# Kernel optimization log

Measured on AMD Instinct MI355X. Metric: run time of the kernel, lower is better.

The kernel has to match this reference:

```python
import jax, jax.numpy as jnp
import numpy as np

N_TYPES = 2
N_NODES = 50000
N_EDGES = 400000
C = 128
H = 4
D = C // H
L = 2
# edge type e connects src node type META[e][0] -> dst node type META[e][1]
META = ((0, 1), (1, 0))


def setup_inputs() -> dict:
    key = jax.random.key(0)
    ks = jax.random.split(key, 16)
    s = 0.05
    return {
        "x": jax.random.normal(ks[0], (N_TYPES, N_NODES, C), jnp.float32),
        "edge_index": jax.random.randint(ks[1], (2, 2, N_EDGES), 0, N_NODES, jnp.int64),
        "Wk": jax.random.normal(ks[2], (L, N_TYPES, C, C), jnp.float32) * s,
        "bk": jax.random.normal(ks[3], (L, N_TYPES, C), jnp.float32) * s,
        "Wq": jax.random.normal(ks[4], (L, N_TYPES, C, C), jnp.float32) * s,
        "bq": jax.random.normal(ks[5], (L, N_TYPES, C), jnp.float32) * s,
        "Wv": jax.random.normal(ks[6], (L, N_TYPES, C, C), jnp.float32) * s,
        "bv": jax.random.normal(ks[7], (L, N_TYPES, C), jnp.float32) * s,
        "Wa": jax.random.normal(ks[8], (L, N_TYPES, C, C), jnp.float32) * s,
        "ba": jax.random.normal(ks[9], (L, N_TYPES, C), jnp.float32) * s,
        "skip": jax.random.normal(ks[10], (L, N_TYPES), jnp.float32),
        "a_rel": jax.random.normal(ks[11], (L, 2, H, D, D), jnp.float32) * s,
        "m_rel": jax.random.normal(ks[12], (L, 2, H, D, D), jnp.float32) * s,
        "p_rel": jnp.ones((L, 2, H), jnp.float32),
        "ln_g": jnp.ones((L, N_TYPES, C), jnp.float32),
        "ln_b": jnp.zeros((L, N_TYPES, C), jnp.float32),
    }


def _layer(x, edge_index, Wk, bk, Wq, bq, Wv, bv, Wa, ba, skip, a_rel, m_rel, p_rel, ln_g, ln_b):
    # x: [T, N, C] ; per-type K/Q/V projections -> [T, N, H, D]
    k = (jnp.einsum('tnc,tcd->tnd', x, Wk) + bk[:, None]).reshape(N_TYPES, N_NODES, H, D)
    q = (jnp.einsum('tnc,tcd->tnd', x, Wq) + bq[:, None]).reshape(N_TYPES, N_NODES, H, D)
    v = (jnp.einsum('tnc,tcd->tnd', x, Wv) + bv[:, None]).reshape(N_TYPES, N_NODES, H, D)
    scale = 1.0 / float(np.sqrt(D))
    out = jnp.zeros((N_TYPES, N_NODES, H, D), x.dtype)
    for e, (st, dt) in enumerate(META):
        si, di = edge_index[e, 0], edge_index[e, 1]
        # per-relation transforms of gathered src keys/values: [E, H, D]
        k_rel = jnp.einsum('ehd,hdf->ehf', k[st][si], a_rel[e])
        v_rel = jnp.einsum('ehd,hdf->ehf', v[st][si], m_rel[e])
        # attention logits [E, H], softmax grouped by destination node
        att = jnp.sum(q[dt][di] * k_rel, axis=-1) * p_rel[e] * scale
        amax = jax.ops.segment_max(att, di, num_segments=N_NODES)
        att = jnp.exp(att - amax[di])
        den = jax.ops.segment_sum(att, di, num_segments=N_NODES)
        att = att / (den[di] + 1e-16)
        agg = jax.ops.segment_sum(att[..., None] * v_rel, di, num_segments=N_NODES)
        out = out.at[dt].add(agg)
    o = out.reshape(N_TYPES, N_NODES, C)
    o = jnp.einsum('tnc,tcd->tnd', jax.nn.gelu(o), Wa) + ba[:, None]
    beta = jax.nn.sigmoid(skip)[:, None, None]
    x = beta * o + (1.0 - beta) * x
    # per-type LayerNorm over features, then ReLU
    mu = jnp.mean(x, axis=-1, keepdims=True)
    var = jnp.var(x, axis=-1, keepdims=True)
    x = (x - mu) * jax.lax.rsqrt(var + 1e-5) * ln_g[:, None] + ln_b[:, None]
    return jax.nn.relu(x)


def reference(x, edge_index, Wk, bk, Wq, bq, Wv, bv, Wa, ba, skip, a_rel, m_rel, p_rel, ln_g, ln_b):
    for l in range(L):
        x = _layer(x, edge_index, Wk[l], bk[l], Wq[l], bq[l], Wv[l], bv[l],
                   Wa[l], ba[l], skip[l], a_rel[l], m_rel[l], p_rel[l], ln_g[l], ln_b[l])
    # x_dict[entity_table]: return node type 0 ("user") embeddings
    return x[0]
```

## Files before the change

### kernel.cpp

```cpp
#include <hip/hip_runtime.h>

#define NN 50000
#define EE 400000
#define CC 128
#define TT 2
#define NT16R 3128
#define KPB 8
#define SCB ((NN + 1023) / 1024)
#define EB ((EE + 256 * KPB - 1) / (256 * KPB))
#define CVTB (NT16R / 4)
#define PREPN (2 * 384 * 128 + 2 * 128 * 128 + 2 * 384)
#define PREPB ((PREPN + 255) / 256)
#define GB ((NN + 31) / 32)

typedef float floatx4 __attribute__((ext_vector_type(4)));
typedef float floatx2 __attribute__((ext_vector_type(2)));
typedef _Float16 half8 __attribute__((ext_vector_type(8)));
typedef _Float16 half2t __attribute__((ext_vector_type(2)));

__device__ __forceinline__ unsigned pk2h(float a, float b) {
    return __builtin_bit_cast(unsigned, __builtin_amdgcn_cvt_pkrtz(a, b));
}
__device__ __forceinline__ float gelu_f(float x) {
    float u = 0.7978845608028654f * (x + 0.044715f * x * x * x);
    float t = __expf(2.f * u);
    return x * (1.f - 1.f / (t + 1.f));
}

__device__ __forceinline__ floatx2 pkfma(floatx2 a, floatx2 b, floatx2 c) {
#if __has_builtin(__builtin_elementwise_fma)
    return __builtin_elementwise_fma(a, b, c);
#else
    floatx2 r;
    r.x = fmaf(a.x, b.x, c.x);
    r.y = fmaf(a.y, b.y, c.y);
    return r;
#endif
}

__device__ __forceinline__ unsigned pk_fp8x4(float a, float b, float c, float d) {
#if __has_builtin(__builtin_amdgcn_cvt_pk_fp8_f32)
    int v = 0;
    v = __builtin_amdgcn_cvt_pk_fp8_f32(a, b, v, false);
    v = __builtin_amdgcn_cvt_pk_fp8_f32(c, d, v, true);
    return (unsigned)v;
#else
    auto enc = [](float x) -> unsigned {
        unsigned u = __float_as_uint(x);
        unsigned s = (u >> 24) & 0x80;
        int e = (int)((u >> 23) & 0xff);
        unsigned m = u & 0x7fffff;
        if (e == 0) return s;
        int ne = e - 127 + 7;
        if (ne <= 0) {
            unsigned full = (1u << 23) | m;
            int sh = 21 - ne;
            if (sh > 24) return s;
            unsigned r = full >> sh;
            unsigned rem = full & ((1u << sh) - 1);
            unsigned half = 1u << (sh - 1);
            if (rem > half || (rem == half && (r & 1))) r++;
            return s | (r & 0x7f);
        }
        unsigned r = m >> 20;
        unsigned rem = m & 0xfffff;
        if (rem > 0x80000 || (rem == 0x80000 && (r & 1))) {
            r++;
            if (r == 8) { r = 0; ne++; }
        }
        if (ne > 15) return s | 0x7e;
        return s | ((unsigned)ne << 3) | r;
    };
    return enc(a) | (enc(b) << 8) | (enc(c) << 16) | (enc(d) << 24);
#endif
}

template <bool HI>
__device__ __forceinline__ floatx2 upk_fp8(unsigned v) {
#if __has_builtin(__builtin_amdgcn_cvt_pk_f32_fp8)
    return __builtin_amdgcn_cvt_pk_f32_fp8((int)v, HI);
#else
    auto dec = [](unsigned b) -> float {
        unsigned s = b & 0x80;
        unsigned e = (b >> 3) & 0xf;
        unsigned m = b & 7;
        float val;
        if (e == 0) val = (float)m * (1.f / 512.f);
        else val = (1.f + (float)m * 0.125f) * exp2f((float)e - 7.f);
        return s ? -val : val;
    };
    unsigned base = HI ? (v >> 16) : v;
    floatx2 r;
    r.x = dec(base & 0xff);
    r.y = dec((base >> 8) & 0xff);
    return r;
#endif
}

__device__ __forceinline__ int detect_is64(const int* __restrict__ ei, int* sflag) {
    if (threadIdx.x == 0) {
        int orv = 0;
#pragma unroll
        for (int i = 1; i < 64; i += 2) orv |= ei[i];
        *sflag = (orv == 0) ? 1 : 0;
    }
    __syncthreads();
    return *sflag;
}

__device__ __forceinline__ void count_body(const int* __restrict__ ei,
                                           int* __restrict__ counts,
                                           unsigned short* __restrict__ rank,
                                           int e, int bx, int* sflag) {
    int is64 = detect_is64(ei, sflag);
    int tid = threadIdx.x;
    int base = bx * (256 * KPB);
    const size_t db = (size_t)(e * 2 + 1) * EE;
    int di[KPB];
    bool val[KPB];
#pragma unroll
    for (int k = 0; k < KPB; k++) {
        int j = base + k * 256 + tid;
        val[k] = j < EE;
        int jc = val[k] ? j : 0;
        int d = is64 ? ei[(db + jc) * 2] : ei[db + jc];
        di[k] = min(max(d, 0), NN - 1);
    }
    int rk[KPB];
#pragma unroll
    for (int k = 0; k < KPB; k++)
        rk[k] = val[k] ? atomicAdd(&counts[e * NN + di[k]], 1) : 0;
#pragma unroll
    for (int k = 0; k < KPB; k++) {
        int j = base + k * 256 + tid;
        if (val[k]) rank[(size_t)e * EE + j] = (unsigned short)rk[k];
    }
}

__device__ __forceinline__ void scatter_body(const int* __restrict__ ei,
                                             const int* __restrict__ rowptr,
                                             const unsigned short* __restrict__ rank,
                                             int* __restrict__ csr,
                                             int e, int bx, int* sflag) {
    int is64 = detect_is64(ei, sflag);
    int tid = threadIdx.x;
    int base = bx * (256 * KPB);
    const size_t sb = (size_t)(e * 2 + 0) * EE;
    const size_t db = (size_t)(e * 2 + 1) * EE;
    int si[KPB], di[KPB], rk[KPB];
#pragma unroll
    for (int k = 0; k < KPB; k++) {
        int j = base + k * 256 + tid;
        int jc = (j < EE) ? j : 0;
        si[k] = is64 ? ei[(sb + jc) * 2] : ei[sb + jc];
        di[k] = is64 ? ei[(db + jc) * 2] : ei[db + jc];
        rk[k] = rank[(size_t)e * EE + jc];
    }
    int pos[KPB];
#pragma unroll
    for (int k = 0; k < KPB; k++) {
        di[k] = min(max(di[k], 0), NN - 1);
        si[k] = min(max(si[k], 0), NN - 1);
    }
#pragma unroll
    for (int k = 0; k < KPB; k++) pos[k] = rowptr[e * (NN + 1) + di[k]] + rk[k];
#pragma unroll
    for (int k = 0; k < KPB; k++) {
        int j = base + k * 256 + tid;
        if (j < EE) csr[(size_t)e * EE + pos[k]] = si[k];
    }
}

__device__ __forceinline__ void cvt_body(const float* __restrict__ x,
                                         _Float16* __restrict__ xs,
                                         int t, int bx, _Float16* sm) {
    int tid = threadIdx.x;
    int node0 = bx * 64;
#pragma unroll
    for (int p = 0; p < 8; p++) {
        int c = p * 256 + tid;
        int row = c >> 5, ch = c & 31;
        int node = min(node0 + row, NN - 1);
        float4 v = *(const float4*)(x + ((size_t)t * NN + node) * CC + ch * 4);
        uint2 o;
        o.x = pk2h(v.x, v.y);
        o.y = pk2h(v.z, v.w);
        *(uint2*)(sm + row * 132 + ch * 4) = o;
    }
    __syncthreads();
    _Float16* xt = xs + (size_t)t * NT16R * 2048;
#pragma unroll
    for (int p = 0; p < 4; p++) {
        int c = p * 256 + tid;
        int tl = c >> 8, kt = (c >> 6) & 3, l = c & 63;
        int q = l >> 4, ln = l & 15;
        *(uint4*)(xt + ((size_t)(bx * 4 + tl) * 4 + kt) * 512 + l * 8) =
            *(const uint4*)(sm + (tl * 16 + ln) * 132 + kt * 32 + q * 8);
    }
}

__device__ __forceinline__ void prep_body(
    const float* __restrict__ Wk, const float* __restrict__ Wq,
    const float* __restrict__ Wv, const float* __restrict__ Wa,
    const float* __restrict__ bk, const float* __restrict__ bq,
    const float* __restrict__ bv,
    const float* __restrict__ a_rel, const float* __restrict__ m_rel,
    const float* __restrict__ p_rel,
    _Float16* __restrict__ W2, _Float16* __restrict__ Wa2,
    float* __restrict__ beff, int l, int idx) {
    const float SCALE = 0.17677669529663687f * 1.4426950408889634f;
    if (idx < 2 * 384 * 128) {
        int t = idx / (384 * 128);
        int r = idx - t * 384 * 128;
        int n = r >> 7, k = r & 127;
        float val;
        if (n < 128) {
            val = Wq[((l * 2 + t) * 128 + k) * 128 + n] *
                  p_rel[(l * 2 + (1 - t)) * 4 + (n >> 5)] * SCALE;
        } else if (n < 256) {
            int nn = n - 128, h = nn >> 5, f = nn & 31;
            const float* wr = Wk + ((l * 2 + t) * 128 + k) * 128 + h * 32;
            const float* ar = a_rel + (((l * 2 + t) * 4 + h) * 32) * 32 + f;
            float s = 0.f;
            for (int d = 0; d < 32; d++) s += wr[d] * ar[d * 32];
            val = s;
        } else {
            int nn = n - 256, h = nn >> 5, f = nn & 31;
            const float* wr = Wv + ((l * 2 + t) * 128 + k) * 128 + h * 32;
            const float* mr = m_rel + (((l * 2 + t) * 4 + h) * 32) * 32 + f;
            float s = 0.f;
            for (int d = 0; d < 32; d++) s += wr[d] * mr[d * 32];
            val = s;
        }
        W2[(((size_t)(l * 2 + t) * 24 + (n >> 4)) * 4 + (k >> 5)) * 512 +
           (((k & 31) >> 3) * 16 + (n & 15)) * 8 + (k & 7)] = (_Float16)val;
    } else if (idx < 2 * 384 * 128 + 2 * 128 * 128) {
        int r = idx - 2 * 384 * 128;
        int t = r / (128 * 128);
        r -= t * 128 * 128;
        int n = r >> 7, k = r & 127;
        float val = Wa[((l * 2 + t) * 128 + k) * 128 + n];
        Wa2[(((size_t)(l * 2 + t) * 8 + (n >> 4)) * 4 + (k >> 5)) * 512 +
            (((k & 31) >> 3) * 16 + (n & 15)) * 8 + (k & 7)] = (_Float16)val;
    } else if (idx < PREPN) {
        int r = idx - (2 * 384 * 128 + 2 * 128 * 128);
        int t = r / 384, n = r - t * 384;
        float val;
        if (n < 128) {
            val = bq[(l * 2 + t) * 128 + n] * p_rel[(l * 2 + (1 - t)) * 4 + (n >> 5)] * SCALE;
        } else if (n < 256) {
            int nn = n - 128, h = nn >> 5, f = nn & 31;
            float s = 0.f;
            for (int d = 0; d < 32; d++)
                s += bk[(l * 2 + t) * 128 + h * 32 + d] *
                     a_rel[(((l * 2 + t) * 4 + h) * 32 + d) * 32 + f];
            val = s;
        } else {
            int nn = n - 256, h = nn >> 5, f = nn & 31;
            float s = 0.f;
            for (int d = 0; d < 32; d++)
                s += bv[(l * 2 + t) * 128 + h * 32 + d] *
                     m_rel[(((l * 2 + t) * 4 + h) * 32 + d) * 32 + f];
            val = s;
        }
        beff[(l * 2 + t) * 384 + n] = val;
    }
}

__global__ __launch_bounds__(256) void k_fuse_pre(
    const int* __restrict__ ei, int* __restrict__ counts,
    unsigned short* __restrict__ rank,
    const float* __restrict__ x, _Float16* __restrict__ xs,
    const float* __restrict__ Wk, const float* __restrict__ Wq,
    const float* __restrict__ Wv, const float* __restrict__ Wa,
    const float* __restrict__ bk, const float* __restrict__ bq,
    const float* __restrict__ bv,
    const float* __restrict__ a_rel, const float* __restrict__ m_rel,
    const float* __restrict__ p_rel,
    _Float16* __restrict__ W2, _Float16* __restrict__ Wa2,
    float* __restrict__ beff) {
    __shared__ _Float16 sm[64 * 132];
    __shared__ int sflag;
    if (blockIdx.x < EB) {
        count_body(ei, counts, rank, blockIdx.y, blockIdx.x, &sflag);
    } else if (blockIdx.x < EB + CVTB) {
        cvt_body(x, xs, blockIdx.y, blockIdx.x - EB, sm);
    } else {
        prep_body(Wk, Wq, Wv, Wa, bk, bq, bv, a_rel, m_rel, p_rel, W2, Wa2, beff,
                  blockIdx.y, (blockIdx.x - EB - CVTB) * 256 + (int)threadIdx.x);
    }
}

__global__ __launch_bounds__(256) void k_scan1(const int* __restrict__ counts,
                                               int* __restrict__ rowptr,
                                               int* __restrict__ bsum) {
    int e = blockIdx.y, b = blockIdx.x;
    int tid = threadIdx.x, lane = tid & 63, wid = tid >> 6;
    __shared__ int wsum[4];
    int base = b * 1024 + tid * 4;
    int v[4], s = 0;
#pragma unroll
    for (int k2 = 0; k2 < 4; k2++) {
        int i = base + k2;
        v[k2] = (i < NN) ? counts[e * NN + i] : 0;
        s += v[k2];
    }
    int incl = s;
#pragma unroll
    for (int off = 1; off < 64; off <<= 1) {
        int t2 = __shfl_up(incl, off);
        if (lane >= off) incl += t2;
    }
    if (lane == 63) wsum[wid] = incl;
    __syncthreads();
    int woff = 0;
    for (int w2 = 0; w2 < wid; w2++) woff += wsum[w2];
    int excl = woff + incl - s;
#pragma unroll
    for (int k2 = 0; k2 < 4; k2++) {
        int i = base + k2;
        if (i < NN) rowptr[e * (NN + 1) + i] = excl;
        excl += v[k2];
    }
    if (tid == 255) bsum[e * SCB + b] = woff + incl;
}

__global__ __launch_bounds__(256) void k_scan23(int* __restrict__ rowptr,
                                                const int* __restrict__ bsum) {
    __shared__ int soff2[2];
    int e = blockIdx.y, b = blockIdx.x;
    int tid = threadIdx.x, lane = tid & 63, wv = tid >> 6;
    if (wv == 0) {
        int v = (lane < SCB) ? bsum[e * SCB + lane] : 0;
        int incl = v;
#pragma unroll
        for (int off = 1; off < 64; off <<= 1) {
            int t2 = __shfl_up(incl, off);
            if (lane >= off) incl += t2;
        }
        if (lane == b) soff2[0] = incl - v;
        if (lane == SCB - 1) soff2[1] = incl;
    }
    __syncthreads();
    int off = soff2[0];
    int base = b * 1024 + tid * 4;
#pragma unroll
    for (int k2 = 0; k2 < 4; k2++) {
        int i = base + k2;
        if (i < NN) rowptr[e * (NN + 1) + i] += off;
    }
    if (b == 0 && tid == 0) rowptr[e * (NN + 1) + NN] = soff2[1];
}

template <int NT, int COL0>
__device__ __forceinline__ void gemm_body(const _Float16* __restrict__ xs,
                                          const _Float16* __restrict__ W2,
                                          const float* __restrict__ beff,
                                          unsigned char* __restrict__ qkv8,
                                          int l, int t, int bx,
                                          unsigned char* tile) {
    constexpr int RB = (NT == 6) ? 512 : 256;
    constexpr int RS = RB + 16;
    int tid = threadIdx.x;
    int wid = tid >> 6, lane = tid & 63;
    int quad = lane >> 4, ln = lane & 15;
    int node0 = bx * 32;
    int tile0 = bx * 2;
    int lt = l * 2 + t;
    const _Float16* Wt = W2 + (size_t)lt * 24 * 2048;
    const _Float16* xt = xs + (size_t)t * NT16R * 2048;
    half8 bf[2][4];
#pragma unroll
    for (int ns = 0; ns < 2; ns++)
#pragma unroll
        for (int kt = 0; kt < 4; kt++)
            bf[ns][kt] = *(const half8*)(xt + ((size_t)(tile0 + ns) * 4 + kt) * 512 + lane * 8);
    floatx4 acc[NT][2];
#pragma unroll
    for (int nt = 0; nt < NT; nt++)
#pragma unroll
        for (int ns = 0; ns < 2; ns++) acc[nt][ns] = (floatx4){0.f, 0.f, 0.f, 0.f};
#pragma unroll
    for (int nt = 0; nt < NT; nt++) {
        int mt = COL0 / 16 + wid * NT + nt;
#pragma unroll
        for (int kt = 0; kt < 4; kt++) {
            half8 af = *(const half8*)(Wt + ((size_t)mt * 4 + kt) * 512 + lane * 8);
            acc[nt][0] = __builtin_amdgcn_mfma_f32_16x16x32_f16(af, bf[0][kt], acc[nt][0], 0, 0, 0);
            acc[nt][1] = __builtin_amdgcn_mfma_f32_16x16x32_f16(af, bf[1][kt], acc[nt][1], 0, 0, 0);
        }
    }
#pragma unroll
    for (int nt = 0; nt < NT; nt++) {
        int c0 = COL0 + wid * NT * 16 + nt * 16 + quad * 4;
        float4 b4 = *(const float4*)(beff + (l * 2 + t) * 384 + c0);
#pragma unroll
        for (int ns = 0; ns < 2; ns++) {
            int nl = ns * 16 + ln;
            float v0 = acc[nt][ns][0] + b4.x, v1 = acc[nt][ns][1] + b4.y;
            float v2 = acc[nt][ns][2] + b4.z, v3 = acc[nt][ns][3] + b4.w;
            unsigned char* rowp = tile + nl * RS;
            if (c0 < 128) {
                uint2 o;
                o.x = pk2h(v0, v1);
                o.y = pk2h(v2, v3);
                *(uint2*)(rowp + 2 * c0) = o;
            } else {
                int f0 = c0 & 127;
                int isV = (c0 >= 256);
                int loff = (f0 >> 3) * 16 + (f0 & 7) + isV * 8 +
                           ((COL0 == 128) ? 0 : 256);
                *(unsigned*)(rowp + loff) = pk_fp8x4(v0, v1, v2, v3);
            }
        }
    }
    __syncthreads();
    constexpr int CPR = RB / 16;
    constexpr int PASSES = (32 * CPR) / 256;
#pragma unroll
    for (int p = 0; p < PASSES; p++) {
        int c = p * 256 + tid;
        int row = c / CPR, ch = c - row * CPR;
        int node = node0 + row;
        if (node < NN)
            *(uint4*)(qkv8 + ((size_t)t * NN + node) * 512 + (COL0 ? 256 : 0) + ch * 16) =
                *(const uint4*)(tile + row * RS + ch * 16);
    }
}

__global__ __launch_bounds__(256) void k_fuse_mid(
    const int* __restrict__ ei, const int* __restrict__ rowptr,
    const unsigned short* __restrict__ rank, int* __restrict__ csr,
    const _Float16* __restrict__ xs, const _Float16* __restrict__ W2,
    const float* __restrict__ beff, unsigned char* __restrict__ qkv8) {
    __shared__ unsigned char tile[32 * 528];
    if (blockIdx.x < EB) {
        scatter_body(ei, rowptr, rank, csr, blockIdx.y, blockIdx.x, (int*)tile);
    } else {
        gemm_body<6, 0>(xs, W2, beff, qkv8, 0, blockIdx.y, blockIdx.x - EB, tile);
    }
}

__global__ __launch_bounds__(256) void k_gemm_l1(const _Float16* __restrict__ xs,
                                                 const _Float16* __restrict__ W2,
                                                 const float* __restrict__ beff,
                                                 unsigned char* __restrict__ qkv8) {
    __shared__ unsigned char tile[32 * 272];
    if (blockIdx.y == 0)
        gemm_body<2, 0>(xs, W2, beff, qkv8, 1, 0, blockIdx.x, tile);
    else
        gemm_body<4, 128>(xs, W2, beff, qkv8, 1, 1, blockIdx.x, tile);
}

__global__ __launch_bounds__(256) void k_attn(const unsigned char* __restrict__ qkv8,
                                              const int* __restrict__ rowptr,
                                              const int* __restrict__ csr,
                                              _Float16* __restrict__ outg) {
    int t = blockIdx.y;
    int e = 1 - t;
    int st = 1 - t;
    int wid = threadIdx.x >> 6, lane = threadIdx.x & 63;
    int n = __builtin_amdgcn_readfirstlane(blockIdx.x * 4 + wid);
    int e4 = lane >> 4, s = lane & 15;
    int r0 = rowptr[e * (NN + 1) + n];
    int r1 = rowptr[e * (NN + 1) + n + 1];
    const int* csrp = csr + (size_t)e * EE;
    const unsigned char* sbase = qkv8 + (size_t)st * NN * 512;
    uint4 qd = *(const uint4*)(qkv8 + ((size_t)t * NN + n) * 512 + s * 16);

    floatx2 acc2[4];
#pragma unroll
    for (int i = 0; i < 4; i++) acc2[i] = (floatx2){0.f, 0.f};
    float lsum = 0.f;
    floatx2 q2[4];

    auto process = [&](const uint4& u, float msk) {
        floatx2 p2 = q2[0] * upk_fp8<false>(u.x);
        p2 = pkfma(q2[1], upk_fp8<true>(u.x), p2);
        p2 = pkfma(q2[2], upk_fp8<false>(u.y), p2);
        p2 = pkfma(q2[3], upk_fp8<true>(u.y), p2);
        float p = p2.x + p2.y;
        p += __shfl_xor(p, 1);
        p += __shfl_xor(p, 2);
        float w = exp2f(p) * msk;
        lsum += w;
        floatx2 w2 = (floatx2){w, w};
        acc2[0] = pkfma(w2, upk_fp8<false>(u.z), acc2[0]);
        acc2[1] = pkfma(w2, upk_fp8<true>(u.z), acc2[1]);
        acc2[2] = pkfma(w2, upk_fp8<false>(u.w), acc2[2]);
        acc2[3] = pkfma(w2, upk_fp8<true>(u.w), acc2[3]);
    };

    if (r0 < r1) {
        int j = r0;
        int iA = csrp[min(j + e4, r1 - 1)];
        int iB = csrp[min(j + 4 + e4, r1 - 1)];
        uint4 uA = (uint4){0u, 0u, 0u, 0u};
        if (j + e4 < r1) uA = *(const uint4*)(sbase + (size_t)iA * 512 + 256 + s * 16);
        {
            half2t h0 = __builtin_bit_cast(half2t, qd.x), h1 = __builtin_bit_cast(half2t, qd.y);
            half2t h2 = __builtin_bit_cast(half2t, qd.z), h3 = __builtin_bit_cast(half2t, qd.w);
            q2[0] = (floatx2){(float)h0.x, (float)h0.y};
            q2[1] = (floatx2){(float)h1.x, (float)h1.y};
            q2[2] = (floatx2){(float)h2.x, (float)h2.y};
            q2[3] = (floatx2){(float)h3.x, (float)h3.y};
        }
        for (; j + 8 < r1; j += 4) {
            uint4 uB = *(const uint4*)(sbase + (size_t)iB * 512 + 256 + s * 16);
            iB = csrp[min(j + 8 + e4, r1 - 1)];
            process(uA, 1.f);
            uA = uB;
        }
        if (j + 4 < r1) {
            uint4 uB = (uint4){0u, 0u, 0u, 0u};
            float mB = (j + 4 + e4 < r1) ? 1.f : 0.f;
            if (j + 4 + e4 < r1)
                uB = *(const uint4*)(sbase + (size_t)iB * 512 + 256 + s * 16);
            process(uA, 1.f);
            process(uB, mB);
        } else {
            process(uA, (j + e4 < r1) ? 1.f : 0.f);
        }
    }
    float accf[8] = {acc2[0].x, acc2[0].y, acc2[1].x, acc2[1].y,
                     acc2[2].x, acc2[2].y, acc2[3].x, acc2[3].y};
#pragma unroll
    for (int i = 0; i < 8; i++) {
        accf[i] += __shfl_xor(accf[i], 16);
        accf[i] += __shfl_xor(accf[i], 32);
    }
    lsum += __shfl_xor(lsum, 16);
    lsum += __shfl_xor(lsum, 32);
    float inv = 1.f / (lsum + 1e-16f);
    if (e4 == 0) {
        uint4 o;
        o.x = pk2h(accf[0] * inv, accf[1] * inv);
        o.y = pk2h(accf[2] * inv, accf[3] * inv);
        o.z = pk2h(accf[4] * inv, accf[5] * inv);
        o.w = pk2h(accf[6] * inv, accf[7] * inv);
        *(uint4*)(outg + ((size_t)t * NN + n) * CC + s * 8) = o;
    }
}

__global__ __launch_bounds__(256) void k_epilogue(
    const _Float16* __restrict__ outg, const _Float16* __restrict__ Wa2,
    const float* __restrict__ ba, const float* __restrict__ skipv,
    const float* __restrict__ ln_g, const float* __restrict__ ln_b,
    const _Float16* __restrict__ xs_cur, _Float16* __restrict__ xs_next,
    float* __restrict__ xout, int l) {
    __shared__ _Float16 smem_h[64 * 132];
    int t = blockIdx.y;
    int tid = threadIdx.x;
    int wid = tid >> 6, lane = tid & 63;
    int quad = lane >> 4, ln = lane & 15;
    int node0 = blockIdx.x * 64;
    int nloc = wid * 16 + ln;
    int node = node0 + nloc;
    int arow = min(node, NN - 1);
    const _Float16* grow = outg + ((size_t)t * NN + arow) * CC;
    uint4 gd4[4];
#pragma unroll
    for (int kt = 0; kt < 4; kt++) gd4[kt] = *(const uint4*)(grow + kt * 32 + quad * 8);
    const _Float16* xt = xs_cur + (size_t)t * NT16R * 2048;
    int tileR = arow >> 4, lnR = arow & 15;
    uint2 xw8[8];
#pragma unroll
    for (int nt = 0; nt < 8; nt++) {
        int c0 = nt * 16 + quad * 4;
        xw8[nt] = *(const uint2*)(xt + ((size_t)tileR * 4 + (c0 >> 5)) * 512 +
                                  (((c0 >> 3) & 3) * 16 + lnR) * 8 + (c0 & 7));
    }
    half8 bf[4];
#pragma unroll
    for (int kt = 0; kt < 4; kt++) {
        uint4 gd = gd4[kt];
        half2t h0 = __builtin_bit_cast(half2t, gd.x), h1 = __builtin_bit_cast(half2t, gd.y);
        half2t h2 = __builtin_bit_cast(half2t, gd.z), h3 = __builtin_bit_cast(half2t, gd.w);
        uint4 pk;
        pk.x = pk2h(gelu_f((float)h0.x), gelu_f((float)h0.y));
        pk.y = pk2h(gelu_f((float)h1.x), gelu_f((float)h1.y));
        pk.z = pk2h(gelu_f((float)h2.x), gelu_f((float)h2.y));
        pk.w = pk2h(gelu_f((float)h3.x), gelu_f((float)h3.y));
        bf[kt] = __builtin_bit_cast(half8, pk);
    }
    const _Float16* Wt = Wa2 + (size_t)(l * 2 + t) * 8 * 2048;
    floatx4 acc[8];
#pragma unroll
    for (int nt = 0; nt < 8; nt++) acc[nt] = (floatx4){0.f, 0.f, 0.f, 0.f};
#pragma unroll
    for (int nt = 0; nt < 8; nt++) {
#pragma unroll
        for (int kt = 0; kt < 4; kt++) {
            half8 af = *(const half8*)(Wt + ((size_t)nt * 4 + kt) * 512 + lane * 8);
            acc[nt] = __builtin_amdgcn_mfma_f32_16x16x32_f16(af, bf[kt], acc[nt], 0, 0, 0);
        }
    }
    float sv = skipv[l * TT + t];
    float beta = 1.f / (1.f + __expf(-sv));
    float xn[8][4];
    float s1 = 0.f, s2 = 0.f;
#pragma unroll
    for (int nt = 0; nt < 8; nt++) {
        int c0 = nt * 16 + quad * 4;
        float4 b4 = *(const float4*)(ba + (l * TT + t) * CC + c0);
        half2t x0 = __builtin_bit_cast(half2t, xw8[nt].x),
               x1 = __builtin_bit_cast(half2t, xw8[nt].y);
        float xv[4] = {(float)x0.x, (float)x0.y, (float)x1.x, (float)x1.y};
        float bb[4] = {b4.x, b4.y, b4.z, b4.w};
#pragma unroll
        for (int reg = 0; reg < 4; reg++) {
            float o = acc[nt][reg] + bb[reg];
            float v = beta * o + (1.f - beta) * xv[reg];
            xn[nt][reg] = v;
            s1 += v;
            s2 += v * v;
        }
    }
    s1 += __shfl_xor(s1, 16); s1 += __shfl_xor(s1, 32);
    s2 += __shfl_xor(s2, 16); s2 += __shfl_xor(s2, 32);
    float mu = s1 * (1.f / CC);
    float var = s2 * (1.f / CC) - mu * mu;
    float rs = rsqrtf(var + 1e-5f);
#pragma unroll
    for (int nt = 0; nt < 8; nt++) {
        int c0 = nt * 16 + quad * 4;
        float4 g4 = *(const float4*)(ln_g + (l * TT + t) * CC + c0);
        float4 be4 = *(const float4*)(ln_b + (l * TT + t) * CC + c0);
        float y0 = fmaxf((xn[nt][0] - mu) * rs * g4.x + be4.x, 0.f);
        float y1 = fmaxf((xn[nt][1] - mu) * rs * g4.y + be4.y, 0.f);
        float y2 = fmaxf((xn[nt][2] - mu) * rs * g4.z + be4.z, 0.f);
        float y3 = fmaxf((xn[nt][3] - mu) * rs * g4.w + be4.w, 0.f);
        if (xout) {
            if (node < NN) {
                float4 o4 = {y0, y1, y2, y3};
                *(float4*)(xout + (size_t)node * CC + c0) = o4;
            }
        } else {
            uint2 o;
            o.x = pk2h(y0, y1);
            o.y = pk2h(y2, y3);
            *(uint2*)(smem_h + nloc * 132 + c0) = o;
        }
    }
    if (!xout) {
        __syncthreads();
        _Float16* xnt = xs_next + (size_t)t * NT16R * 2048;
#pragma unroll
        for (int p = 0; p < 4; p++) {
            int c = p * 256 + tid;
            int tl = c >> 8, kt2 = (c >> 6) & 3, l2 = c & 63;
            int q2 = l2 >> 4, ln2 = l2 & 15;
            *(uint4*)(xnt + ((size_t)(blockIdx.x * 4 + tl) * 4 + kt2) * 512 + l2 * 8) =
                *(const uint4*)(smem_h + (tl * 16 + ln2) * 132 + kt2 * 32 + q2 * 8);
        }
    }
}

extern "C" void kernel_launch(void* const* d_in, const int* in_sizes, int n_in,
                              void* d_out, int out_size, void* d_ws, size_t ws_size,
                              hipStream_t stream) {
    const float* x = (const float*)d_in[0];
    const int* ei = (const int*)d_in[1];
    const float* Wk = (const float*)d_in[2];
    const float* bk = (const float*)d_in[3];
    const float* Wq = (const float*)d_in[4];
    const float* bq = (const float*)d_in[5];
    const float* Wv = (const float*)d_in[6];
    const float* bv = (const float*)d_in[7];
    const float* Wa = (const float*)d_in[8];
    const float* ba = (const float*)d_in[9];
    const float* skip = (const float*)d_in[10];
    const float* a_rel = (const float*)d_in[11];
    const float* m_rel = (const float*)d_in[12];
    const float* p_rel = (const float*)d_in[13];
    const float* ln_g = (const float*)d_in[14];
    const float* ln_b = (const float*)d_in[15];

    char* ws = (char*)d_ws;
    size_t off = 0;
    auto alloc = [&](size_t b) {
        size_t o = off;
        off = (off + b + 255) & ~(size_t)255;
        return o;
    };
    _Float16* xsA = (_Float16*)(ws + alloc((size_t)TT * NT16R * 2048 * 2));
    _Float16* xsB = (_Float16*)(ws + alloc((size_t)TT * NT16R * 2048 * 2));
    unsigned char* qkv8 = (unsigned char*)(ws + alloc((size_t)TT * NN * 512));
    _Float16* outg = (_Float16*)(ws + alloc((size_t)TT * NN * CC * 2));
    _Float16* W2 = (_Float16*)(ws + alloc((size_t)2 * TT * 24 * 2048 * 2));
    _Float16* Wa2 = (_Float16*)(ws + alloc((size_t)2 * TT * 8 * 2048 * 2));
    float* beff = (float*)(ws + alloc((size_t)2 * TT * 384 * 4));
    int* counts = (int*)(ws + alloc((size_t)2 * NN * 4));
    unsigned short* rankb = (unsigned short*)(ws + alloc((size_t)2 * EE * 2));
    int* rowptr = (int*)(ws + alloc((size_t)2 * (NN + 1) * 4));
    int* csr = (int*)(ws + alloc((size_t)2 * EE * 4));
    int* bsum = (int*)(ws + alloc((size_t)2 * SCB * 4 + 256));
    (void)ws_size; (void)in_sizes; (void)n_in; (void)out_size;

    (void)hipMemsetAsync(counts, 0, (size_t)2 * NN * 4, stream);
    k_fuse_pre<<<dim3(EB + CVTB + PREPB, 2), 256, 0, stream>>>(
        ei, counts, rankb, x, xsA, Wk, Wq, Wv, Wa, bk, bq, bv, a_rel, m_rel,
        p_rel, W2, Wa2, beff);
    k_scan1<<<dim3(SCB, 2), 256, 0, stream>>>(counts, rowptr, bsum);
    k_scan23<<<dim3(SCB, 2), 256, 0, stream>>>(rowptr, bsum);
    k_fuse_mid<<<dim3(EB + GB, 2), 256, 0, stream>>>(
        ei, rowptr, rankb, csr, xsA, W2, beff, qkv8);
    k_attn<<<dim3(NN / 4, 2), 256, 0, stream>>>(qkv8, rowptr, csr, outg);
    k_epilogue<<<dim3((NN + 63) / 64, 2), 256, 0, stream>>>(
        outg, Wa2, ba, skip, ln_g, ln_b, xsA, xsB, nullptr, 0);
    k_gemm_l1<<<dim3(GB, 2), 256, 0, stream>>>(xsB, W2, beff, qkv8);
    k_attn<<<dim3(NN / 4, 1), 256, 0, stream>>>(qkv8, rowptr, csr, outg);
    k_epilogue<<<dim3((NN + 63) / 64, 1), 256, 0, stream>>>(
        outg, Wa2, ba, skip, ln_g, ln_b, xsB, nullptr, (float*)d_out, 1);
}
```

Baseline: 308.3 us.

## Count destination degrees with per-block LDS histograms over node ranges

Edge degree counting now gives each block a 2048-node range of destinations. Every block scans all edges, bumps LDS atomics only for destinations in its range, and writes its counts out directly. This removes global atomics and the memset of the counts buffer. In exchange, each of the 25 blocks per edge type reads the whole 400k-entry destination array, about 25x redundant reads, with few blocks active, which may lengthen the critical path of the fused pre-kernel.

```diff
diff --git a/kernel.cpp b/kernel.cpp
--- a/kernel.cpp
+++ b/kernel.cpp
@@ -6,6 +6,9 @@
 #define TT 2
 #define NT16R 3128
 #define KPB 8
+#define KPC 16
+#define BINS 2048
+#define CNTB ((NN + BINS - 1) / BINS)
 #define SCB ((NN + 1023) / 1024)
 #define EB ((EE + 256 * KPB - 1) / (256 * KPB))
 #define CVTB (NT16R / 4)
@@ -111,29 +114,37 @@
 __device__ __forceinline__ void count_body(const int* __restrict__ ei,
                                            int* __restrict__ counts,
                                            unsigned short* __restrict__ rank,
-                                           int e, int bx, int* sflag) {
+                                           int e, int bx, int* bins, int* sflag) {
+    int tid = threadIdx.x;
+    for (int i = tid; i < BINS; i += 256) bins[i] = 0;
     int is64 = detect_is64(ei, sflag);
-    int tid = threadIdx.x;
-    int base = bx * (256 * KPB);
+    int base = bx * BINS;
     const size_t db = (size_t)(e * 2 + 1) * EE;
-    int di[KPB];
-    bool val[KPB];
-#pragma unroll
-    for (int k = 0; k < KPB; k++) {
-        int j = base + k * 256 + tid;
-        val[k] = j < EE;
-        int jc = val[k] ? j : 0;
-        int d = is64 ? ei[(db + jc) * 2] : ei[db + jc];
-        di[k] = min(max(d, 0), NN - 1);
-    }
-    int rk[KPB];
-#pragma unroll
-    for (int k = 0; k < KPB; k++)
-        rk[k] = val[k] ? atomicAdd(&counts[e * NN + di[k]], 1) : 0;
-#pragma unroll
-    for (int k = 0; k < KPB; k++) {
-        int j = base + k * 256 + tid;
-        if (val[k]) rank[(size_t)e * EE + j] = (unsigned short)rk[k];
+    for (int it = 0; it < EE; it += 256 * KPC) {
+        int d[KPC];
+        bool ok[KPC];
+#pragma unroll
+        for (int k = 0; k < KPC; k++) {
+            int j = it + k * 256 + tid;
+            ok[k] = j < EE;
+            int jc = ok[k] ? j : 0;
+            int dd = is64 ? ei[(db + jc) * 2] : ei[db + jc];
+            d[k] = min(max(dd, 0), NN - 1);
+        }
+#pragma unroll
+        for (int k = 0; k < KPC; k++) {
+            int j = it + k * 256 + tid;
+            int local = d[k] - base;
+            if (ok[k] && local >= 0 && local < BINS) {
+                int r = atomicAdd(&bins[local], 1);
+                rank[(size_t)e * EE + j] = (unsigned short)r;
+            }
+        }
+    }
+    __syncthreads();
+    for (int i = tid; i < BINS; i += 256) {
+        int g = base + i;
+        if (g < NN) counts[e * NN + g] = bins[i];
     }
 }
 
@@ -279,15 +290,15 @@
     const float* __restrict__ p_rel,
     _Float16* __restrict__ W2, _Float16* __restrict__ Wa2,
     float* __restrict__ beff) {
-    __shared__ _Float16 sm[64 * 132];
+    __shared__ int sbuf[4224];
     __shared__ int sflag;
-    if (blockIdx.x < EB) {
-        count_body(ei, counts, rank, blockIdx.y, blockIdx.x, &sflag);
-    } else if (blockIdx.x < EB + CVTB) {
-        cvt_body(x, xs, blockIdx.y, blockIdx.x - EB, sm);
+    if (blockIdx.x < CNTB) {
+        count_body(ei, counts, rank, blockIdx.y, blockIdx.x, sbuf, &sflag);
+    } else if (blockIdx.x < CNTB + CVTB) {
+        cvt_body(x, xs, blockIdx.y, blockIdx.x - CNTB, (_Float16*)sbuf);
     } else {
         prep_body(Wk, Wq, Wv, Wa, bk, bq, bv, a_rel, m_rel, p_rel, W2, Wa2, beff,
-                  blockIdx.y, (blockIdx.x - EB - CVTB) * 256 + (int)threadIdx.x);
+                  blockIdx.y, (blockIdx.x - CNTB - CVTB) * 256 + (int)threadIdx.x);
     }
 }
 
@@ -697,8 +708,7 @@
     int* bsum = (int*)(ws + alloc((size_t)2 * SCB * 4 + 256));
     (void)ws_size; (void)in_sizes; (void)n_in; (void)out_size;
 
-    (void)hipMemsetAsync(counts, 0, (size_t)2 * NN * 4, stream);
-    k_fuse_pre<<<dim3(EB + CVTB + PREPB, 2), 256, 0, stream>>>(
+    k_fuse_pre<<<dim3(CNTB + CVTB + PREPB, 2), 256, 0, stream>>>(
         ei, counts, rankb, x, xsA, Wk, Wq, Wv, Wa, bk, bq, bv, a_rel, m_rel,
         p_rel, W2, Wa2, beff);
     k_scan1<<<dim3(SCB, 2), 256, 0, stream>>>(counts, rowptr, bsum);
```

New measurement: 431.8 us. 1.4x slower.
